# Optimization experiments

Hardware: AMD Instinct MI355X
Metric: run time of the kernel (lower is better)

Reference implementation:

```python
import jax, jax.numpy as jnp
import numpy as np

VQ_NUM = 3
EMB_NUM = 1024
COMMITMENT_WEIGHT = 1.0
# cumprod of [1, emb_num, emb_num] -> per-stage index bases
CUMPROD = [1, EMB_NUM, EMB_NUM * EMB_NUM]


def setup_inputs() -> dict:
    key = jax.random.key(0)
    k0, k1, k2, k3 = jax.random.split(key, 4)
    z = jax.random.normal(k0, (8, 4096, 512), dtype=jnp.float32)
    # linear_in: nn.Linear(in_ch=512, emb_ch=256, bias=False) -> weight [emb_ch, in_ch]
    W_in = jax.random.normal(k1, (VQ_NUM, 256, 512), dtype=jnp.float32) * 0.02
    # linear_out: nn.Linear(emb_ch=256, in_ch=512, bias=False) -> weight [in_ch, emb_ch]
    W_out = jax.random.normal(k2, (VQ_NUM, 512, 256), dtype=jnp.float32) * 0.02
    # one codebook per stage (share_residual_codebooks=False)
    codebooks = jax.random.normal(k3, (VQ_NUM, EMB_NUM, 256), dtype=jnp.float32) * 0.02
    return {"z": z, "W_in": W_in, "W_out": W_out, "codebooks": codebooks}


def reference(z, W_in, W_out, codebooks):
    sg = jax.lax.stop_gradient
    z_q = jnp.zeros_like(z)
    r = z
    loss = jnp.float32(0.0)
    index_sum = jnp.zeros(z.shape[:2], dtype=jnp.int64 if jax.config.jax_enable_x64 else jnp.int32)
    for i in range(VQ_NUM):
        # linear_in
        zi = jnp.einsum('bnc,ec->bne', r, W_in[i])  # [B,N,emb_ch]
        v = codebooks[i]  # [S, emb_ch]
        # squared L2 distance: ||z||^2 + ||v||^2 - 2 z.v
        dist = (jnp.sum(zi * zi, axis=-1, keepdims=True)
                + jnp.sum(v * v, axis=-1)
                - 2.0 * jnp.einsum('bne,se->bns', zi, v))  # [B,N,S]
        idx = jnp.argmin(dist, axis=-1)  # [B,N] int
        zq = v[idx]  # codebook lookup, [B,N,emb_ch]
        loss = loss + (COMMITMENT_WEIGHT * jnp.mean((sg(zq) - zi) ** 2)
                       + jnp.mean((zq - sg(zi)) ** 2))
        # straight-through estimator
        zq_ste = zi + sg(zq - zi)
        # linear_out
        r_q = jnp.einsum('bne,ce->bnc', zq_ste, W_out[i])  # [B,N,in_ch]
        index_sum = index_sum + idx.astype(index_sum.dtype) * CUMPROD[i]
        z_q = z_q + r_q
        r = z - sg(z_q)
    loss = loss / VQ_NUM + jnp.mean((z_q - z) ** 2)
    return z_q, index_sum, loss
```

## Files before the change

### kernel.cpp

```cpp
#include <hip/hip_runtime.h>

#define MTOK 32768
#define CIN  512
#define EMB  256
#define NCODE 1024
#define VQ   3
#define DELTA 2e-3f

typedef short s16x8 __attribute__((ext_vector_type(8)));
typedef float f32x4 __attribute__((ext_vector_type(4)));
typedef unsigned short u16;

static __device__ __forceinline__ u16 f2bf(float x) {
    unsigned int u = __float_as_uint(x);
    u += 0x7FFF + ((u >> 16) & 1);
    return (u16)(u >> 16);
}
static __device__ __forceinline__ float bf2f(u16 h) {
    return __uint_as_float(((unsigned int)h) << 16);
}

__global__ void init_k(double* loss_acc, int* cnt) {
    loss_acc[0] = 0.0;
    loss_acc[1] = 0.0;
    #pragma unroll
    for (int i = 0; i < 8; ++i) cnt[i] = 0;
}

__global__ __launch_bounds__(64) void prep_cb_k(const float* __restrict__ cbs,
                                                double* __restrict__ vnorm64,
                                                float* __restrict__ vnorm32,
                                                u16* __restrict__ cbh,
                                                u16* __restrict__ cbl) {
    int s = blockIdx.x;
    const float* row = cbs + (size_t)s * EMB;
    double acc = 0.0;
    for (int k = threadIdx.x; k < EMB; k += 64) {
        float v = row[k];
        double vd = (double)v; acc += vd * vd;
        u16 h = f2bf(v);
        u16 l = f2bf(v - bf2f(h));
        cbh[(size_t)s * EMB + k] = h;
        cbl[(size_t)s * EMB + k] = l;
    }
    #pragma unroll
    for (int off = 32; off > 0; off >>= 1) acc += __shfl_down(acc, off, 64);
    if (threadIdx.x == 0) { vnorm64[s] = acc; vnorm32[s] = (float)acc; }
}

__global__ __launch_bounds__(256) void prep_w_k(const float* __restrict__ W_in,
                                                u16* __restrict__ wh,
                                                u16* __restrict__ wl) {
    int i = blockIdx.x * 256 + threadIdx.x;
    float v = W_in[i];
    u16 h = f2bf(v);
    wh[i] = h;
    wl[i] = f2bf(v - bf2f(h));
}

__global__ __launch_bounds__(256) void prep_wt_k(const float* __restrict__ W_in,
                                                 float* __restrict__ WinT) {
    int i = blockIdx.x * 256 + threadIdx.x;
    int s = i / (EMB * CIN);
    int rem = i - s * (EMB * CIN);
    int e = rem / CIN;
    int k = rem - e * CIN;
    WinT[(size_t)s * CIN * EMB + (size_t)k * EMB + e] = W_in[i];
}

__global__ __launch_bounds__(256) void prep_T_k(const float* __restrict__ cbs,
                                                const float* __restrict__ Wout,
                                                float* __restrict__ T) {
    const int stage = blockIdx.z;
    const float* A = cbs  + (size_t)stage * NCODE * EMB;
    const float* B = Wout + (size_t)stage * CIN * EMB;
    float* C = T + (size_t)stage * NCODE * CIN;
    __shared__ float As[64][33];
    __shared__ float Bs[64][33];
    const int tid = threadIdx.x;
    const int ty = tid >> 4, tx = tid & 15;
    const int m0 = blockIdx.x * 64;
    const int n0 = blockIdx.y * 64;
    const int lrow = tid >> 5, lcol = tid & 31;
    double acc[4][4];
    #pragma unroll
    for (int i = 0; i < 4; ++i)
        #pragma unroll
        for (int j = 0; j < 4; ++j) acc[i][j] = 0.0;

    for (int k0 = 0; k0 < EMB; k0 += 32) {
        __syncthreads();
        #pragma unroll
        for (int t = 0; t < 8; ++t) {
            int r = lrow + 8 * t;
            As[r][lcol] = A[(size_t)(m0 + r) * EMB + k0 + lcol];
            Bs[r][lcol] = B[(size_t)(n0 + r) * EMB + k0 + lcol];
        }
        __syncthreads();
        #pragma unroll
        for (int k = 0; k < 32; ++k) {
            double a[4], b[4];
            #pragma unroll
            for (int i = 0; i < 4; ++i) a[i] = (double)As[ty * 4 + i][k];
            #pragma unroll
            for (int j = 0; j < 4; ++j) b[j] = (double)Bs[tx * 4 + j][k];
            #pragma unroll
            for (int i = 0; i < 4; ++i)
                #pragma unroll
                for (int j = 0; j < 4; ++j) acc[i][j] += a[i] * b[j];
        }
    }
    #pragma unroll
    for (int i = 0; i < 4; ++i) {
        float4 v = make_float4((float)acc[i][0], (float)acc[i][1],
                               (float)acc[i][2], (float)acc[i][3]);
        *reinterpret_cast<float4*>(&C[(size_t)(m0 + ty * 4 + i) * CIN + n0 + tx * 4]) = v;
    }
}

__global__ __launch_bounds__(256, 2) void zi_mfma_k(const float* __restrict__ z,
                                                    const float* __restrict__ zq,
                                                    const u16* __restrict__ wh,
                                                    const u16* __restrict__ wl,
                                                    float* __restrict__ zi,
                                                    double* __restrict__ loss_acc,
                                                    int stage0) {
    __shared__ __align__(16) u16 swh[2][16][520];
    __shared__ __align__(16) u16 swl[2][16][520];
    const int tid = threadIdx.x;
    const int w = tid >> 6;
    const int l = tid & 63;
    const int col = l & 15;
    const int g = l >> 4;
    const int mw = blockIdx.x * 64 + w * 16;
    const int sr = tid >> 4, sq = tid & 15;

    s16x8 ah[16], al[16];
    {
        const float* zr = z  + (size_t)(mw + col) * CIN + g * 8;
        const float* qr = zq + (size_t)(mw + col) * CIN + g * 8;
        #pragma unroll
        for (int kc = 0; kc < 16; ++kc) {
            float4 f0 = *reinterpret_cast<const float4*>(zr + kc * 32);
            float4 f1 = *reinterpret_cast<const float4*>(zr + kc * 32 + 4);
            float f[8] = {f0.x, f0.y, f0.z, f0.w, f1.x, f1.y, f1.z, f1.w};
            if (!stage0) {
                float4 q0 = *reinterpret_cast<const float4*>(qr + kc * 32);
                float4 q1 = *reinterpret_cast<const float4*>(qr + kc * 32 + 4);
                f[0] -= q0.x; f[1] -= q0.y; f[2] -= q0.z; f[3] -= q0.w;
                f[4] -= q1.x; f[5] -= q1.y; f[6] -= q1.z; f[7] -= q1.w;
            }
            #pragma unroll
            for (int j = 0; j < 8; ++j) {
                u16 h = f2bf(f[j]);
                u16 lo = f2bf(f[j] - bf2f(h));
                ah[kc][j] = (short)h; al[kc][j] = (short)lo;
            }
        }
    }

    const u16* gh = wh + (size_t)sr * CIN + sq * 8;
    const u16* gl = wl + (size_t)sr * CIN + sq * 8;
    uint4 h0, h1, h2, h3, l0, l1, l2, l3;
#define ZLOAD(NT) do { const u16* th = gh + (size_t)(NT) * (16 * CIN);                \
    const u16* tl = gl + (size_t)(NT) * (16 * CIN);                                   \
    h0 = *(const uint4*)(th);        h1 = *(const uint4*)(th + 128);                  \
    h2 = *(const uint4*)(th + 256);  h3 = *(const uint4*)(th + 384);                  \
    l0 = *(const uint4*)(tl);        l1 = *(const uint4*)(tl + 128);                  \
    l2 = *(const uint4*)(tl + 256);  l3 = *(const uint4*)(tl + 384); } while (0)
#define ZWRITE(P) do {                                                                \
    *(uint4*)&swh[P][sr][sq * 8]       = h0;  *(uint4*)&swh[P][sr][sq * 8 + 128] = h1;\
    *(uint4*)&swh[P][sr][sq * 8 + 256] = h2;  *(uint4*)&swh[P][sr][sq * 8 + 384] = h3;\
    *(uint4*)&swl[P][sr][sq * 8]       = l0;  *(uint4*)&swl[P][sr][sq * 8 + 128] = l1;\
    *(uint4*)&swl[P][sr][sq * 8 + 256] = l2;  *(uint4*)&swl[P][sr][sq * 8 + 384] = l3;\
    } while (0)
    ZLOAD(0); ZWRITE(0); ZLOAD(1);

    double zn = 0.0;
    for (int nt = 0; nt < 16; ++nt) {
        __syncthreads();
        const int p = nt & 1;
        if (nt + 1 < 16) ZWRITE((nt + 1) & 1);
        if (nt + 2 < 16) ZLOAD(nt + 2);
        f32x4 a0 = {0.f, 0.f, 0.f, 0.f};
        f32x4 a1 = {0.f, 0.f, 0.f, 0.f};
        f32x4 a2 = {0.f, 0.f, 0.f, 0.f};
        #pragma unroll
        for (int kc = 0; kc < 16; ++kc) {
            s16x8 Bh = *(const s16x8*)&swh[p][col][g * 8 + kc * 32];
            s16x8 Bl = *(const s16x8*)&swl[p][col][g * 8 + kc * 32];
            a0 = __builtin_amdgcn_mfma_f32_16x16x32_bf16(ah[kc], Bh, a0, 0, 0, 0);
            a1 = __builtin_amdgcn_mfma_f32_16x16x32_bf16(al[kc], Bh, a1, 0, 0, 0);
            a2 = __builtin_amdgcn_mfma_f32_16x16x32_bf16(ah[kc], Bl, a2, 0, 0, 0);
        }
        #pragma unroll
        for (int r = 0; r < 4; ++r) {
            float v = a0[r] + a1[r] + a2[r];
            zi[(size_t)(mw + g * 4 + r) * EMB + nt * 16 + col] = v;
            zn += (double)v * (double)v;
        }
    }
#undef ZLOAD
#undef ZWRITE
    #pragma unroll
    for (int off = 32; off > 0; off >>= 1) zn += __shfl_down(zn, off, 64);
    if (l == 0) atomicAdd(loss_acc, zn);
}

__global__ __launch_bounds__(256, 2) void pref_k(const float* __restrict__ zi,
                                                 const u16* __restrict__ cbh,
                                                 const u16* __restrict__ cbl,
                                                 const float* __restrict__ vnorm32,
                                                 int* __restrict__ idx,
                                                 int* __restrict__ idx_sum,
                                                 float* __restrict__ mind,
                                                 int* __restrict__ flagged,
                                                 int* __restrict__ cnt,
                                                 int* __restrict__ fullList,
                                                 int* __restrict__ cntF,
                                                 int* __restrict__ cand2,
                                                 double* __restrict__ loss_acc,
                                                 int stage0, int cumprod) {
    __shared__ __align__(16) u16 sbh[2][16][264];
    __shared__ __align__(16) u16 sbl[2][16][264];
    __shared__ double loss_s[16];
    const int tid = threadIdx.x;
    const int w = tid >> 6;
    const int l = tid & 63;
    const int col = l & 15;
    const int g = l >> 4;
    const int mw = blockIdx.x * 64 + w * 16;
    const int sr = tid >> 4, sq = tid & 15;

    s16x8 ah[8], al[8];
    {
        const float* zr = zi + (size_t)(mw + col) * EMB + g * 8;
        #pragma unroll
        for (int kc = 0; kc < 8; ++kc) {
            float4 f0 = *reinterpret_cast<const float4*>(zr + kc * 32);
            float4 f1 = *reinterpret_cast<const float4*>(zr + kc * 32 + 4);
            float f[8] = {f0.x, f0.y, f0.z, f0.w, f1.x, f1.y, f1.z, f1.w};
            #pragma unroll
            for (int j = 0; j < 8; ++j) {
                u16 h = f2bf(f[j]);
                u16 lo = f2bf(f[j] - bf2f(h));
                ah[kc][j] = (short)h;
                al[kc][j] = (short)lo;
            }
        }
    }

    float b1[4] = {1e30f, 1e30f, 1e30f, 1e30f};
    float b2[4] = {1e30f, 1e30f, 1e30f, 1e30f};
    float b3[4] = {1e30f, 1e30f, 1e30f, 1e30f};
    int   i1[4] = {0, 0, 0, 0};
    int   i2[4] = {0, 0, 0, 0};

    const u16* gh = cbh + (size_t)sr * EMB + sq * 8;
    const u16* gl = cbl + (size_t)sr * EMB + sq * 8;
    uint4 h0, h1, l0, l1;
#define PLOAD(CT) do { const u16* th = gh + (size_t)(CT) * (16 * EMB);                \
    const u16* tl = gl + (size_t)(CT) * (16 * EMB);                                   \
    h0 = *(const uint4*)(th);  h1 = *(const uint4*)(th + 128);                        \
    l0 = *(const uint4*)(tl);  l1 = *(const uint4*)(tl + 128); } while (0)
#define PWRITE(P) do {                                                                \
    *(uint4*)&sbh[P][sr][sq * 8] = h0;  *(uint4*)&sbh[P][sr][sq * 8 + 128] = h1;      \
    *(uint4*)&sbl[P][sr][sq * 8] = l0;  *(uint4*)&sbl[P][sr][sq * 8 + 128] = l1;      \
    } while (0)
    PLOAD(0); PWRITE(0); PLOAD(1);

    for (int ct = 0; ct < 64; ++ct) {
        __syncthreads();
        const int p = ct & 1;
        if (ct + 1 < 64) PWRITE((ct + 1) & 1);
        if (ct + 2 < 64) PLOAD(ct + 2);
        const float vn = vnorm32[ct * 16 + col];
        f32x4 a0 = {0.f, 0.f, 0.f, 0.f};
        f32x4 a1 = {0.f, 0.f, 0.f, 0.f};
        f32x4 a2 = {0.f, 0.f, 0.f, 0.f};
        #pragma unroll
        for (int kc = 0; kc < 8; ++kc) {
            s16x8 Bh = *(const s16x8*)&sbh[p][col][g * 8 + kc * 32];
            s16x8 Bl = *(const s16x8*)&sbl[p][col][g * 8 + kc * 32];
            a0 = __builtin_amdgcn_mfma_f32_16x16x32_bf16(ah[kc], Bh, a0, 0, 0, 0);
            a1 = __builtin_amdgcn_mfma_f32_16x16x32_bf16(al[kc], Bh, a1, 0, 0, 0);
            a2 = __builtin_amdgcn_mfma_f32_16x16x32_bf16(ah[kc], Bl, a2, 0, 0, 0);
        }
        #pragma unroll
        for (int r = 0; r < 4; ++r) {
            float sc = vn - 2.f * (a0[r] + a1[r] + a2[r]);
            int c = ct * 16 + col;
            if (sc < b1[r]) { b3[r] = b2[r]; b2[r] = b1[r]; i2[r] = i1[r]; b1[r] = sc; i1[r] = c; }
            else if (sc < b2[r]) { b3[r] = b2[r]; b2[r] = sc; i2[r] = c; }
            else b3[r] = fminf(b3[r], sc);
        }
    }
#undef PLOAD
#undef PWRITE

    #pragma unroll
    for (int off = 1; off < 16; off <<= 1) {
        #pragma unroll
        for (int r = 0; r < 4; ++r) {
            float c1 = __shfl_xor(b1[r], off, 64);
            int   j1 = __shfl_xor(i1[r], off, 64);
            float c2 = __shfl_xor(b2[r], off, 64);
            int   j2 = __shfl_xor(i2[r], off, 64);
            float c3 = __shfl_xor(b3[r], off, 64);
            float nb1, nb2, nb3; int ni1, ni2;
            if (c1 < b1[r] || (c1 == b1[r] && j1 < i1[r])) {
                nb1 = c1; ni1 = j1;
                if (b1[r] < c2 || (b1[r] == c2 && i1[r] < j2)) {
                    nb2 = b1[r]; ni2 = i1[r]; nb3 = fminf(b2[r], c2);
                } else {
                    nb2 = c2; ni2 = j2; nb3 = fminf(b1[r], c3);
                }
            } else {
                nb1 = b1[r]; ni1 = i1[r];
                if (c1 < b2[r] || (c1 == b2[r] && j1 < i2[r])) {
                    nb2 = c1; ni2 = j1; nb3 = fminf(b2[r], c2);
                } else {
                    nb2 = b2[r]; ni2 = i2[r]; nb3 = fminf(c1, b3[r]);
                }
            }
            b1[r] = nb1; b2[r] = nb2; b3[r] = nb3; i1[r] = ni1; i2[r] = ni2;
        }
    }
    if (col == 0) {
        double lsum = 0.0;
        #pragma unroll
        for (int r = 0; r < 4; ++r) {
            int m = mw + g * 4 + r;
            idx[m] = i1[r];
            if (stage0) idx_sum[m] = i1[r];
            else        idx_sum[m] += i1[r] * cumprod;
            mind[m] = b1[r];
            lsum += (double)b1[r];
            if (b2[r] - b1[r] < DELTA) {
                if (b3[r] - b1[r] < DELTA) {
                    int slot = atomicAdd(cntF, 1);
                    fullList[slot] = m;
                } else {
                    int slot = atomicAdd(cnt, 1);
                    flagged[slot] = m;
                    cand2[m] = i2[r];
                }
            }
        }
        loss_s[w * 4 + g] = lsum;
    }
    __syncthreads();
    if (tid == 0) {
        double s = 0.0;
        #pragma unroll
        for (int q = 0; q < 16; ++q) s += loss_s[q];
        atomicAdd(loss_acc, s);
    }
}

__global__ __launch_bounds__(256) void rescan_pair_k(const float* __restrict__ z,
                                                     const float* __restrict__ zqv,
                                                     const float* __restrict__ WinT,
                                                     const float* __restrict__ cb,
                                                     const double* __restrict__ vnorm64,
                                                     const int* __restrict__ flagged,
                                                     const int* __restrict__ cnt,
                                                     const int* __restrict__ cand2,
                                                     int* __restrict__ idx,
                                                     int* __restrict__ idx_sum,
                                                     float* __restrict__ mind,
                                                     double* __restrict__ loss_acc,
                                                     int cumprod, int stage0) {
    __shared__ double r64[8][CIN];
    __shared__ int mArr[8], cAArr[8], cBArr[8];
    double* zi_l = &r64[0][0];
    const int tid = threadIdx.x;
    const int w = tid >> 6, l = tid & 63;
    const int n = *cnt;

    for (int jb = blockIdx.x; jb * 8 < n; jb += gridDim.x) {
        const int nt = min(8, n - jb * 8);
        __syncthreads();
        if (tid < nt) {
            int m = flagged[jb * 8 + tid];
            mArr[tid] = m;
            cAArr[tid] = idx[m]; cBArr[tid] = cand2[m];
        }
        __syncthreads();
        for (int t = 0; t < nt; ++t) {
            const int m = mArr[t];
            #pragma unroll
            for (int h = 0; h < 2; ++h) {
                int k = tid + h * 256;
                float rv = z[(size_t)m * CIN + k];
                if (!stage0) rv -= zqv[(size_t)m * CIN + k];
                r64[t][k] = (double)rv;
            }
        }
        __syncthreads();
        double acc[8] = {0, 0, 0, 0, 0, 0, 0, 0};
        #pragma unroll 4
        for (int k = 0; k < CIN; ++k) {
            double wv = (double)WinT[(size_t)k * EMB + tid];
            #pragma unroll
            for (int t = 0; t < 8; ++t) acc[t] += r64[t][k] * wv;
        }
        __syncthreads();
        #pragma unroll
        for (int t = 0; t < 8; ++t) zi_l[t * 256 + tid] = acc[t];
        __syncthreads();

        for (int t = w; t < nt; t += 4) {
            const int cA = cAArr[t], cB = cBArr[t], m = mArr[t];
            const double* zt = zi_l + t * 256;
            float4 vA = *(const float4*)(cb + (size_t)cA * EMB + 4 * l);
            float4 vB = *(const float4*)(cb + (size_t)cB * EMB + 4 * l);
            double z0 = zt[4 * l], z1 = zt[4 * l + 1];
            double z2 = zt[4 * l + 2], z3 = zt[4 * l + 3];
            double sA = z0 * (double)vA.x + z1 * (double)vA.y
                      + z2 * (double)vA.z + z3 * (double)vA.w;
            double sB = z0 * (double)vB.x + z1 * (double)vB.y
                      + z2 * (double)vB.z + z3 * (double)vB.w;
            #pragma unroll
            for (int off = 1; off < 64; off <<= 1) {
                sA += __shfl_xor(sA, off, 64);
                sB += __shfl_xor(sB, off, 64);
            }
            if (l == 0) {
                double dA = vnorm64[cA] - 2.0 * sA;
                double dB = vnorm64[cB] - 2.0 * sB;
                int bi; double best;
                if (dB < dA || (dB == dA && cB < cA)) { bi = cB; best = dB; }
                else                                   { bi = cA; best = dA; }
                int oldI = idx[m];
                if (bi != oldI) { idx[m] = bi; idx_sum[m] += (bi - oldI) * cumprod; }
                atomicAdd(loss_acc, best - (double)mind[m]);
                mind[m] = (float)best;
            }
        }
    }
}

__global__ __launch_bounds__(256) void fullscan_k(const float* __restrict__ z,
                                                  const float* __restrict__ zqv,
                                                  const float* __restrict__ WinT,
                                                  const float* __restrict__ cb,
                                                  const double* __restrict__ vnorm64,
                                                  const int* __restrict__ fullList,
                                                  const int* __restrict__ cntF,
                                                  int* __restrict__ idx,
                                                  int* __restrict__ idx_sum,
                                                  float* __restrict__ mind,
                                                  double* __restrict__ loss_acc,
                                                  int cumprod, int stage0) {
    __shared__ double r64[CIN];
    __shared__ double zi64[EMB];
    __shared__ double sred[256];
    __shared__ int ired[256];
    const int tid = threadIdx.x;
    const int n = *cntF;

    for (int j = blockIdx.x; j < n; j += gridDim.x) {
        const int m = fullList[j];
        __syncthreads();
        #pragma unroll
        for (int h = 0; h < 2; ++h) {
            int k = tid + h * 256;
            float rv = z[(size_t)m * CIN + k];
            if (!stage0) rv -= zqv[(size_t)m * CIN + k];
            r64[k] = (double)rv;
        }
        __syncthreads();
        {
            double acc = 0.0;
            #pragma unroll 8
            for (int k = 0; k < CIN; ++k)
                acc += r64[k] * (double)WinT[(size_t)k * EMB + tid];
            zi64[tid] = acc;
        }
        __syncthreads();
        double best = 1e300; int bi = 0;
        #pragma unroll
        for (int q = 0; q < 4; ++q) {
            const int c = q * 256 + tid;
            const float* row = cb + (size_t)c * EMB;
            double s0 = 0, s1 = 0, s2 = 0, s3 = 0;
            #pragma unroll 4
            for (int e = 0; e < EMB; e += 4) {
                float4 v = *(const float4*)(row + e);
                s0 += zi64[e]     * (double)v.x;
                s1 += zi64[e + 1] * (double)v.y;
                s2 += zi64[e + 2] * (double)v.z;
                s3 += zi64[e + 3] * (double)v.w;
            }
            double sc = vnorm64[c] - 2.0 * ((s0 + s1) + (s2 + s3));
            if (sc < best) { best = sc; bi = c; }
        }
        sred[tid] = best; ired[tid] = bi;
        __syncthreads();
        for (int off = 128; off > 0; off >>= 1) {
            if (tid < off) {
                double ob = sred[tid + off]; int oi = ired[tid + off];
                if (ob < sred[tid] || (ob == sred[tid] && oi < ired[tid])) {
                    sred[tid] = ob; ired[tid] = oi;
                }
            }
            __syncthreads();
        }
        if (tid == 0) {
            int oldI = idx[m], bi2 = ired[0];
            double best2 = sred[0];
            if (bi2 != oldI) { idx[m] = bi2; idx_sum[m] += (bi2 - oldI) * cumprod; }
            atomicAdd(loss_acc, best2 - (double)mind[m]);
            mind[m] = (float)best2;
        }
    }
}

__global__ __launch_bounds__(256) void gather_k(const float* __restrict__ T,
                                                const int* __restrict__ idx,
                                                const float* __restrict__ z,
                                                float* __restrict__ zq,
                                                int stage0, int last,
                                                double* __restrict__ loss_acc) {
    __shared__ double red[256];
    int m = blockIdx.x * 16 + (threadIdx.x >> 4);
    int q = threadIdx.x & 15;
    const float* src = T + (size_t)idx[m] * CIN;
    float* dst = zq + (size_t)m * CIN;
    double s = 0.0;
    #pragma unroll
    for (int it = 0; it < 8; ++it) {
        int off = it * 64 + q * 4;
        float4 t = *reinterpret_cast<const float4*>(src + off);
        if (!stage0) {
            float4 o = *reinterpret_cast<const float4*>(dst + off);
            t.x += o.x; t.y += o.y; t.z += o.z; t.w += o.w;
        }
        *reinterpret_cast<float4*>(dst + off) = t;
        if (last) {
            float4 zv = *reinterpret_cast<const float4*>(z + (size_t)m * CIN + off);
            double d0 = (double)zv.x - (double)t.x;
            double d1 = (double)zv.y - (double)t.y;
            double d2 = (double)zv.z - (double)t.z;
            double d3 = (double)zv.w - (double)t.w;
            s += d0 * d0 + d1 * d1 + d2 * d2 + d3 * d3;
        }
    }
    if (last) {
        red[threadIdx.x] = s;
        __syncthreads();
        for (int off = 128; off > 0; off >>= 1) {
            if (threadIdx.x < off) red[threadIdx.x] += red[threadIdx.x + off];
            __syncthreads();
        }
        if (threadIdx.x == 0) atomicAdd(loss_acc + 1, red[0]);
    }
}

__global__ void final_k(const int* __restrict__ idx_sum,
                        const double* __restrict__ loss_acc,
                        float* __restrict__ out) {
    int i = blockIdx.x * blockDim.x + threadIdx.x;
    if (i < MTOK) out[MTOK * CIN + i] = (float)idx_sum[i];
    if (i == 0) {
        double loss = 2.0 * loss_acc[0] / (3.0 * (double)MTOK * (double)EMB)
                    + loss_acc[1] / ((double)MTOK * (double)CIN);
        out[MTOK * CIN + MTOK] = (float)loss;
    }
}

extern "C" void kernel_launch(void* const* d_in, const int* in_sizes, int n_in,
                              void* d_out, int out_size, void* d_ws, size_t ws_size,
                              hipStream_t stream) {
    const float* z     = (const float*)d_in[0];
    const float* W_in  = (const float*)d_in[1];
    const float* W_out = (const float*)d_in[2];
    const float* cbs   = (const float*)d_in[3];
    float* out = (float*)d_out;
    char* ws = (char*)d_ws;

    double* vnorm64  = (double*)ws;
    double* loss_acc = (double*)(ws + 24576);
    int*    cnt      = (int*)(ws + 24592);
    float*  vnorm32  = (float*)(ws + 24624);
    u16*    cbh      = (u16*)(ws + 36912);
    u16*    cbl      = (u16*)(ws + 1609776);
    u16*    wh       = (u16*)(ws + 3182640);
    u16*    wl       = (u16*)(ws + 3969072);
    float*  WinT     = (float*)(ws + 4755504);
    float*  T        = (float*)(ws + 6328368);
    float*  zi       = (float*)(ws + 12619824);
    char*   p        = ws + 46174256;
    int*    idx      = (int*)p;
    int*    idx_sum  = (int*)(p + 131072);
    int*    flagged  = (int*)(p + 262144);
    float*  mind     = (float*)(p + 393216);
    int*    cand2    = (int*)(p + 524288);
    int*    fullList = (int*)(p + 655360);

    float* zq = out;

    init_k<<<dim3(1), dim3(1), 0, stream>>>(loss_acc, cnt);
    prep_cb_k<<<dim3(VQ * NCODE), dim3(64), 0, stream>>>(cbs, vnorm64, vnorm32, cbh, cbl);
    prep_w_k<<<dim3(VQ * EMB * CIN / 256), dim3(256), 0, stream>>>(W_in, wh, wl);
    prep_wt_k<<<dim3(VQ * EMB * CIN / 256), dim3(256), 0, stream>>>(W_in, WinT);
    prep_T_k<<<dim3(NCODE / 64, CIN / 64, VQ), dim3(256), 0, stream>>>(cbs, W_out, T);

    const int cumprod[VQ] = {1, 1024, 1024 * 1024};
    for (int i = 0; i < VQ; ++i) {
        const float* cb = cbs + (size_t)i * NCODE * EMB;
        zi_mfma_k<<<dim3(MTOK / 64), dim3(256), 0, stream>>>(
            z, zq, wh + (size_t)i * EMB * CIN, wl + (size_t)i * EMB * CIN,
            zi, loss_acc, i == 0 ? 1 : 0);
        pref_k<<<dim3(MTOK / 64), dim3(256), 0, stream>>>(
            zi, cbh + (size_t)i * NCODE * EMB, cbl + (size_t)i * NCODE * EMB,
            vnorm32 + i * NCODE, idx, idx_sum, mind, flagged, cnt + i,
            fullList, cnt + 3 + i, cand2, loss_acc, i == 0 ? 1 : 0, cumprod[i]);
        rescan_pair_k<<<dim3(512), dim3(256), 0, stream>>>(
            z, zq, WinT + (size_t)i * EMB * CIN, cb, vnorm64 + i * NCODE,
            flagged, cnt + i, cand2, idx, idx_sum, mind, loss_acc, cumprod[i],
            i == 0 ? 1 : 0);
        fullscan_k<<<dim3(256), dim3(256), 0, stream>>>(
            z, zq, WinT + (size_t)i * EMB * CIN, cb, vnorm64 + i * NCODE,
            fullList, cnt + 3 + i, idx, idx_sum, mind, loss_acc, cumprod[i],
            i == 0 ? 1 : 0);
        gather_k<<<dim3(MTOK / 16), dim3(256), 0, stream>>>(
            T + (size_t)i * NCODE * CIN, idx, z, zq, i == 0 ? 1 : 0,
            i == VQ - 1 ? 1 : 0, loss_acc);
    }
    final_k<<<dim3(MTOK / 256), dim3(256), 0, stream>>>(idx_sum, loss_acc, out);
}
```

Before: 936.4 us.

## Process two 16-row token tiles per wave in pref_k to reuse codebook tiles

```diff
diff --git a/kernel.cpp b/kernel.cpp
--- a/kernel.cpp
+++ b/kernel.cpp
@@ -207,7 +207,7 @@
     if (l == 0) atomicAdd(loss_acc, zn);
 }
 
-__global__ __launch_bounds__(256, 2) void pref_k(const float* __restrict__ zi,
+__global__ __launch_bounds__(256, 1) void pref_k(const float* __restrict__ zi,
                                                  const u16* __restrict__ cbh,
                                                  const u16* __restrict__ cbl,
                                                  const float* __restrict__ vnorm32,
@@ -229,32 +229,45 @@
     const int l = tid & 63;
     const int col = l & 15;
     const int g = l >> 4;
-    const int mw = blockIdx.x * 64 + w * 16;
+    const int mw = blockIdx.x * 128 + w * 32;
     const int sr = tid >> 4, sq = tid & 15;
 
-    s16x8 ah[8], al[8];
+    s16x8 ah0[8], al0[8], ah1[8], al1[8];
     {
-        const float* zr = zi + (size_t)(mw + col) * EMB + g * 8;
+        const float* zr0 = zi + (size_t)(mw + col) * EMB + g * 8;
+        const float* zr1 = zi + (size_t)(mw + 16 + col) * EMB + g * 8;
         #pragma unroll
         for (int kc = 0; kc < 8; ++kc) {
-            float4 f0 = *reinterpret_cast<const float4*>(zr + kc * 32);
-            float4 f1 = *reinterpret_cast<const float4*>(zr + kc * 32 + 4);
+            float4 f0 = *reinterpret_cast<const float4*>(zr0 + kc * 32);
+            float4 f1 = *reinterpret_cast<const float4*>(zr0 + kc * 32 + 4);
             float f[8] = {f0.x, f0.y, f0.z, f0.w, f1.x, f1.y, f1.z, f1.w};
             #pragma unroll
             for (int j = 0; j < 8; ++j) {
                 u16 h = f2bf(f[j]);
                 u16 lo = f2bf(f[j] - bf2f(h));
-                ah[kc][j] = (short)h;
-                al[kc][j] = (short)lo;
-            }
-        }
-    }
-
-    float b1[4] = {1e30f, 1e30f, 1e30f, 1e30f};
-    float b2[4] = {1e30f, 1e30f, 1e30f, 1e30f};
-    float b3[4] = {1e30f, 1e30f, 1e30f, 1e30f};
-    int   i1[4] = {0, 0, 0, 0};
-    int   i2[4] = {0, 0, 0, 0};
+                ah0[kc][j] = (short)h;
+                al0[kc][j] = (short)lo;
+            }
+            float4 e0 = *reinterpret_cast<const float4*>(zr1 + kc * 32);
+            float4 e1 = *reinterpret_cast<const float4*>(zr1 + kc * 32 + 4);
+            float e[8] = {e0.x, e0.y, e0.z, e0.w, e1.x, e1.y, e1.z, e1.w};
+            #pragma unroll
+            for (int j = 0; j < 8; ++j) {
+                u16 h = f2bf(e[j]);
+                u16 lo = f2bf(e[j] - bf2f(h));
+                ah1[kc][j] = (short)h;
+                al1[kc][j] = (short)lo;
+            }
+        }
+    }
+
+    float b1a[4], b2a[4], b3a[4], b1b[4], b2b[4], b3b[4];
+    int   i1a[4], i2a[4], i1b[4], i2b[4];
+    #pragma unroll
+    for (int r = 0; r < 4; ++r) {
+        b1a[r] = b2a[r] = b3a[r] = 1e30f; i1a[r] = i2a[r] = 0;
+        b1b[r] = b2b[r] = b3b[r] = 1e30f; i1b[r] = i2b[r] = 0;
+    }
 
     const u16* gh = cbh + (size_t)sr * EMB + sq * 8;
     const u16* gl = cbl + (size_t)sr * EMB + sq * 8;
@@ -275,75 +288,103 @@
         if (ct + 1 < 64) PWRITE((ct + 1) & 1);
         if (ct + 2 < 64) PLOAD(ct + 2);
         const float vn = vnorm32[ct * 16 + col];
-        f32x4 a0 = {0.f, 0.f, 0.f, 0.f};
-        f32x4 a1 = {0.f, 0.f, 0.f, 0.f};
-        f32x4 a2 = {0.f, 0.f, 0.f, 0.f};
+        f32x4 a00 = {0.f, 0.f, 0.f, 0.f}, a01 = {0.f, 0.f, 0.f, 0.f}, a02 = {0.f, 0.f, 0.f, 0.f};
+        f32x4 a10 = {0.f, 0.f, 0.f, 0.f}, a11 = {0.f, 0.f, 0.f, 0.f}, a12 = {0.f, 0.f, 0.f, 0.f};
         #pragma unroll
         for (int kc = 0; kc < 8; ++kc) {
             s16x8 Bh = *(const s16x8*)&sbh[p][col][g * 8 + kc * 32];
             s16x8 Bl = *(const s16x8*)&sbl[p][col][g * 8 + kc * 32];
-            a0 = __builtin_amdgcn_mfma_f32_16x16x32_bf16(ah[kc], Bh, a0, 0, 0, 0);
-            a1 = __builtin_amdgcn_mfma_f32_16x16x32_bf16(al[kc], Bh, a1, 0, 0, 0);
-            a2 = __builtin_amdgcn_mfma_f32_16x16x32_bf16(ah[kc], Bl, a2, 0, 0, 0);
+            a00 = __builtin_amdgcn_mfma_f32_16x16x32_bf16(ah0[kc], Bh, a00, 0, 0, 0);
+            a10 = __builtin_amdgcn_mfma_f32_16x16x32_bf16(ah1[kc], Bh, a10, 0, 0, 0);
+            a01 = __builtin_amdgcn_mfma_f32_16x16x32_bf16(al0[kc], Bh, a01, 0, 0, 0);
+            a11 = __builtin_amdgcn_mfma_f32_16x16x32_bf16(al1[kc], Bh, a11, 0, 0, 0);
+            a02 = __builtin_amdgcn_mfma_f32_16x16x32_bf16(ah0[kc], Bl, a02, 0, 0, 0);
+            a12 = __builtin_amdgcn_mfma_f32_16x16x32_bf16(ah1[kc], Bl, a12, 0, 0, 0);
         }
         #pragma unroll
         for (int r = 0; r < 4; ++r) {
-            float sc = vn - 2.f * (a0[r] + a1[r] + a2[r]);
             int c = ct * 16 + col;
-            if (sc < b1[r]) { b3[r] = b2[r]; b2[r] = b1[r]; i2[r] = i1[r]; b1[r] = sc; i1[r] = c; }
-            else if (sc < b2[r]) { b3[r] = b2[r]; b2[r] = sc; i2[r] = c; }
-            else b3[r] = fminf(b3[r], sc);
+            float sa = vn - 2.f * (a00[r] + a01[r] + a02[r]);
+            if (sa < b1a[r]) { b3a[r] = b2a[r]; b2a[r] = b1a[r]; i2a[r] = i1a[r]; b1a[r] = sa; i1a[r] = c; }
+            else if (sa < b2a[r]) { b3a[r] = b2a[r]; b2a[r] = sa; i2a[r] = c; }
+            else b3a[r] = fminf(b3a[r], sa);
+            float sb = vn - 2.f * (a10[r] + a11[r] + a12[r]);
+            if (sb < b1b[r]) { b3b[r] = b2b[r]; b2b[r] = b1b[r]; i2b[r] = i1b[r]; b1b[r] = sb; i1b[r] = c; }
+            else if (sb < b2b[r]) { b3b[r] = b2b[r]; b2b[r] = sb; i2b[r] = c; }
+            else b3b[r] = fminf(b3b[r], sb);
         }
     }
 #undef PLOAD
 #undef PWRITE
 
-    #pragma unroll
-    for (int off = 1; off < 16; off <<= 1) {
-        #pragma unroll
-        for (int r = 0; r < 4; ++r) {
-            float c1 = __shfl_xor(b1[r], off, 64);
-            int   j1 = __shfl_xor(i1[r], off, 64);
-            float c2 = __shfl_xor(b2[r], off, 64);
-            int   j2 = __shfl_xor(i2[r], off, 64);
-            float c3 = __shfl_xor(b3[r], off, 64);
-            float nb1, nb2, nb3; int ni1, ni2;
-            if (c1 < b1[r] || (c1 == b1[r] && j1 < i1[r])) {
-                nb1 = c1; ni1 = j1;
-                if (b1[r] < c2 || (b1[r] == c2 && i1[r] < j2)) {
-                    nb2 = b1[r]; ni2 = i1[r]; nb3 = fminf(b2[r], c2);
-                } else {
-                    nb2 = c2; ni2 = j2; nb3 = fminf(b1[r], c3);
-                }
-            } else {
-                nb1 = b1[r]; ni1 = i1[r];
-                if (c1 < b2[r] || (c1 == b2[r] && j1 < i2[r])) {
-                    nb2 = c1; ni2 = j1; nb3 = fminf(b2[r], c2);
-                } else {
-                    nb2 = b2[r]; ni2 = i2[r]; nb3 = fminf(c1, b3[r]);
-                }
-            }
-            b1[r] = nb1; b2[r] = nb2; b3[r] = nb3; i1[r] = ni1; i2[r] = ni2;
-        }
-    }
+#define MERGE16(B1, B2, B3, I1, I2) do {                                              \
+    _Pragma("unroll")                                                                 \
+    for (int off = 1; off < 16; off <<= 1) {                                          \
+        _Pragma("unroll")                                                             \
+        for (int r = 0; r < 4; ++r) {                                                 \
+            float c1 = __shfl_xor(B1[r], off, 64);                                    \
+            int   j1 = __shfl_xor(I1[r], off, 64);                                    \
+            float c2 = __shfl_xor(B2[r], off, 64);                                    \
+            int   j2 = __shfl_xor(I2[r], off, 64);                                    \
+            float c3 = __shfl_xor(B3[r], off, 64);                                    \
+            float nb1, nb2, nb3; int ni1, ni2;                                        \
+            if (c1 < B1[r] || (c1 == B1[r] && j1 < I1[r])) {                          \
+                nb1 = c1; ni1 = j1;                                                   \
+                if (B1[r] < c2 || (B1[r] == c2 && I1[r] < j2)) {                      \
+                    nb2 = B1[r]; ni2 = I1[r]; nb3 = fminf(B2[r], c2);                 \
+                } else {                                                              \
+                    nb2 = c2; ni2 = j2; nb3 = fminf(B1[r], c3);                       \
+                }                                                                     \
+            } else {                                                                  \
+                nb1 = B1[r]; ni1 = I1[r];                                             \
+                if (c1 < B2[r] || (c1 == B2[r] && j1 < I2[r])) {                      \
+                    nb2 = c1; ni2 = j1; nb3 = fminf(B2[r], c2);                       \
+                } else {                                                              \
+                    nb2 = B2[r]; ni2 = I2[r]; nb3 = fminf(c1, B3[r]);                 \
+                }                                                                     \
+            }                                                                         \
+            B1[r] = nb1; B2[r] = nb2; B3[r] = nb3; I1[r] = ni1; I2[r] = ni2;          \
+        }                                                                             \
+    }                                                                                 \
+} while (0)
+    MERGE16(b1a, b2a, b3a, i1a, i2a);
+    MERGE16(b1b, b2b, b3b, i1b, i2b);
+#undef MERGE16
+
     if (col == 0) {
         double lsum = 0.0;
         #pragma unroll
         for (int r = 0; r < 4; ++r) {
             int m = mw + g * 4 + r;
-            idx[m] = i1[r];
-            if (stage0) idx_sum[m] = i1[r];
-            else        idx_sum[m] += i1[r] * cumprod;
-            mind[m] = b1[r];
-            lsum += (double)b1[r];
-            if (b2[r] - b1[r] < DELTA) {
-                if (b3[r] - b1[r] < DELTA) {
+            idx[m] = i1a[r];
+            if (stage0) idx_sum[m] = i1a[r];
+            else        idx_sum[m] += i1a[r] * cumprod;
+            mind[m] = b1a[r];
+            lsum += (double)b1a[r];
+            if (b2a[r] - b1a[r] < DELTA) {
+                if (b3a[r] - b1a[r] < DELTA) {
                     int slot = atomicAdd(cntF, 1);
                     fullList[slot] = m;
                 } else {
                     int slot = atomicAdd(cnt, 1);
                     flagged[slot] = m;
-                    cand2[m] = i2[r];
+                    cand2[m] = i2a[r];
+                }
+            }
+            int m2 = mw + 16 + g * 4 + r;
+            idx[m2] = i1b[r];
+            if (stage0) idx_sum[m2] = i1b[r];
+            else        idx_sum[m2] += i1b[r] * cumprod;
+            mind[m2] = b1b[r];
+            lsum += (double)b1b[r];
+            if (b2b[r] - b1b[r] < DELTA) {
+                if (b3b[r] - b1b[r] < DELTA) {
+                    int slot = atomicAdd(cntF, 1);
+                    fullList[slot] = m2;
+                } else {
+                    int slot = atomicAdd(cnt, 1);
+                    flagged[slot] = m2;
+                    cand2[m2] = i2b[r];
                 }
             }
         }
@@ -613,7 +654,7 @@
         zi_mfma_k<<<dim3(MTOK / 64), dim3(256), 0, stream>>>(
             z, zq, wh + (size_t)i * EMB * CIN, wl + (size_t)i * EMB * CIN,
             zi, loss_acc, i == 0 ? 1 : 0);
-        pref_k<<<dim3(MTOK / 64), dim3(256), 0, stream>>>(
+        pref_k<<<dim3(MTOK / 128), dim3(256), 0, stream>>>(
             zi, cbh + (size_t)i * NCODE * EMB, cbl + (size_t)i * NCODE * EMB,
             vnorm32 + i * NCODE, idx, idx_sum, mind, flagged, cnt + i,
             fullList, cnt + 3 + i, cand2, loss_acc, i == 0 ? 1 : 0, cumprod[i]);
```

After: 1.028 ms. 1.1x slower.

## Fuse linear_in MFMA projection into codebook prefilter kernel with packed bf16 split

Applied to the files above, without the earlier changes.

```diff
diff --git a/kernel.cpp b/kernel.cpp
--- a/kernel.cpp
+++ b/kernel.cpp
@@ -10,6 +10,7 @@
 typedef short s16x8 __attribute__((ext_vector_type(8)));
 typedef float f32x4 __attribute__((ext_vector_type(4)));
 typedef unsigned short u16;
+typedef unsigned int u32;
 
 static __device__ __forceinline__ u16 f2bf(float x) {
     unsigned int u = __float_as_uint(x);
@@ -118,109 +119,24 @@
     }
 }
 
-__global__ __launch_bounds__(256, 2) void zi_mfma_k(const float* __restrict__ z,
-                                                    const float* __restrict__ zq,
-                                                    const u16* __restrict__ wh,
-                                                    const u16* __restrict__ wl,
-                                                    float* __restrict__ zi,
-                                                    double* __restrict__ loss_acc,
-                                                    int stage0) {
-    __shared__ __align__(16) u16 swh[2][16][520];
-    __shared__ __align__(16) u16 swl[2][16][520];
-    const int tid = threadIdx.x;
-    const int w = tid >> 6;
-    const int l = tid & 63;
-    const int col = l & 15;
-    const int g = l >> 4;
-    const int mw = blockIdx.x * 64 + w * 16;
-    const int sr = tid >> 4, sq = tid & 15;
-
-    s16x8 ah[16], al[16];
-    {
-        const float* zr = z  + (size_t)(mw + col) * CIN + g * 8;
-        const float* qr = zq + (size_t)(mw + col) * CIN + g * 8;
-        #pragma unroll
-        for (int kc = 0; kc < 16; ++kc) {
-            float4 f0 = *reinterpret_cast<const float4*>(zr + kc * 32);
-            float4 f1 = *reinterpret_cast<const float4*>(zr + kc * 32 + 4);
-            float f[8] = {f0.x, f0.y, f0.z, f0.w, f1.x, f1.y, f1.z, f1.w};
-            if (!stage0) {
-                float4 q0 = *reinterpret_cast<const float4*>(qr + kc * 32);
-                float4 q1 = *reinterpret_cast<const float4*>(qr + kc * 32 + 4);
-                f[0] -= q0.x; f[1] -= q0.y; f[2] -= q0.z; f[3] -= q0.w;
-                f[4] -= q1.x; f[5] -= q1.y; f[6] -= q1.z; f[7] -= q1.w;
-            }
-            #pragma unroll
-            for (int j = 0; j < 8; ++j) {
-                u16 h = f2bf(f[j]);
-                u16 lo = f2bf(f[j] - bf2f(h));
-                ah[kc][j] = (short)h; al[kc][j] = (short)lo;
-            }
-        }
-    }
-
-    const u16* gh = wh + (size_t)sr * CIN + sq * 8;
-    const u16* gl = wl + (size_t)sr * CIN + sq * 8;
-    uint4 h0, h1, h2, h3, l0, l1, l2, l3;
-#define ZLOAD(NT) do { const u16* th = gh + (size_t)(NT) * (16 * CIN);                \
-    const u16* tl = gl + (size_t)(NT) * (16 * CIN);                                   \
-    h0 = *(const uint4*)(th);        h1 = *(const uint4*)(th + 128);                  \
-    h2 = *(const uint4*)(th + 256);  h3 = *(const uint4*)(th + 384);                  \
-    l0 = *(const uint4*)(tl);        l1 = *(const uint4*)(tl + 128);                  \
-    l2 = *(const uint4*)(tl + 256);  l3 = *(const uint4*)(tl + 384); } while (0)
-#define ZWRITE(P) do {                                                                \
-    *(uint4*)&swh[P][sr][sq * 8]       = h0;  *(uint4*)&swh[P][sr][sq * 8 + 128] = h1;\
-    *(uint4*)&swh[P][sr][sq * 8 + 256] = h2;  *(uint4*)&swh[P][sr][sq * 8 + 384] = h3;\
-    *(uint4*)&swl[P][sr][sq * 8]       = l0;  *(uint4*)&swl[P][sr][sq * 8 + 128] = l1;\
-    *(uint4*)&swl[P][sr][sq * 8 + 256] = l2;  *(uint4*)&swl[P][sr][sq * 8 + 384] = l3;\
-    } while (0)
-    ZLOAD(0); ZWRITE(0); ZLOAD(1);
-
-    double zn = 0.0;
-    for (int nt = 0; nt < 16; ++nt) {
-        __syncthreads();
-        const int p = nt & 1;
-        if (nt + 1 < 16) ZWRITE((nt + 1) & 1);
-        if (nt + 2 < 16) ZLOAD(nt + 2);
-        f32x4 a0 = {0.f, 0.f, 0.f, 0.f};
-        f32x4 a1 = {0.f, 0.f, 0.f, 0.f};
-        f32x4 a2 = {0.f, 0.f, 0.f, 0.f};
-        #pragma unroll
-        for (int kc = 0; kc < 16; ++kc) {
-            s16x8 Bh = *(const s16x8*)&swh[p][col][g * 8 + kc * 32];
-            s16x8 Bl = *(const s16x8*)&swl[p][col][g * 8 + kc * 32];
-            a0 = __builtin_amdgcn_mfma_f32_16x16x32_bf16(ah[kc], Bh, a0, 0, 0, 0);
-            a1 = __builtin_amdgcn_mfma_f32_16x16x32_bf16(al[kc], Bh, a1, 0, 0, 0);
-            a2 = __builtin_amdgcn_mfma_f32_16x16x32_bf16(ah[kc], Bl, a2, 0, 0, 0);
-        }
-        #pragma unroll
-        for (int r = 0; r < 4; ++r) {
-            float v = a0[r] + a1[r] + a2[r];
-            zi[(size_t)(mw + g * 4 + r) * EMB + nt * 16 + col] = v;
-            zn += (double)v * (double)v;
-        }
-    }
-#undef ZLOAD
-#undef ZWRITE
-    #pragma unroll
-    for (int off = 32; off > 0; off >>= 1) zn += __shfl_down(zn, off, 64);
-    if (l == 0) atomicAdd(loss_acc, zn);
-}
-
-__global__ __launch_bounds__(256, 2) void pref_k(const float* __restrict__ zi,
-                                                 const u16* __restrict__ cbh,
-                                                 const u16* __restrict__ cbl,
-                                                 const float* __restrict__ vnorm32,
-                                                 int* __restrict__ idx,
-                                                 int* __restrict__ idx_sum,
-                                                 float* __restrict__ mind,
-                                                 int* __restrict__ flagged,
-                                                 int* __restrict__ cnt,
-                                                 int* __restrict__ fullList,
-                                                 int* __restrict__ cntF,
-                                                 int* __restrict__ cand2,
-                                                 double* __restrict__ loss_acc,
-                                                 int stage0, int cumprod) {
+__global__ __launch_bounds__(256, 2) void fused_k(const float* __restrict__ z,
+                                                  const float* __restrict__ zq,
+                                                  const u16* __restrict__ wh,
+                                                  const u16* __restrict__ wl,
+                                                  const u16* __restrict__ cbh,
+                                                  const u16* __restrict__ cbl,
+                                                  const float* __restrict__ vnorm32,
+                                                  u32* __restrict__ zi_hl,
+                                                  int* __restrict__ idx,
+                                                  int* __restrict__ idx_sum,
+                                                  float* __restrict__ mind,
+                                                  int* __restrict__ flagged,
+                                                  int* __restrict__ cnt,
+                                                  int* __restrict__ fullList,
+                                                  int* __restrict__ cntF,
+                                                  int* __restrict__ cand2,
+                                                  double* __restrict__ loss_acc,
+                                                  int stage0, int cumprod) {
     __shared__ __align__(16) u16 sbh[2][16][264];
     __shared__ __align__(16) u16 sbl[2][16][264];
     __shared__ double loss_s[16];
@@ -232,20 +148,95 @@
     const int mw = blockIdx.x * 64 + w * 16;
     const int sr = tid >> 4, sq = tid & 15;
 
-    s16x8 ah[8], al[8];
     {
-        const float* zr = zi + (size_t)(mw + col) * EMB + g * 8;
-        #pragma unroll
-        for (int kc = 0; kc < 8; ++kc) {
+        s16x8 ah[16], al[16];
+        const float* zr = z  + (size_t)(mw + col) * CIN + g * 8;
+        const float* qr = zq + (size_t)(mw + col) * CIN + g * 8;
+        #pragma unroll
+        for (int kc = 0; kc < 16; ++kc) {
             float4 f0 = *reinterpret_cast<const float4*>(zr + kc * 32);
             float4 f1 = *reinterpret_cast<const float4*>(zr + kc * 32 + 4);
             float f[8] = {f0.x, f0.y, f0.z, f0.w, f1.x, f1.y, f1.z, f1.w};
+            if (!stage0) {
+                float4 q0 = *reinterpret_cast<const float4*>(qr + kc * 32);
+                float4 q1 = *reinterpret_cast<const float4*>(qr + kc * 32 + 4);
+                f[0] -= q0.x; f[1] -= q0.y; f[2] -= q0.z; f[3] -= q0.w;
+                f[4] -= q1.x; f[5] -= q1.y; f[6] -= q1.z; f[7] -= q1.w;
+            }
             #pragma unroll
             for (int j = 0; j < 8; ++j) {
                 u16 h = f2bf(f[j]);
                 u16 lo = f2bf(f[j] - bf2f(h));
-                ah[kc][j] = (short)h;
-                al[kc][j] = (short)lo;
+                ah[kc][j] = (short)h; al[kc][j] = (short)lo;
+            }
+        }
+
+        const u16* gwh = wh + (size_t)sr * CIN + sq * 8;
+        const u16* gwl = wl + (size_t)sr * CIN + sq * 8;
+        uint4 h0, h1, h2, h3, l0, l1, l2, l3;
+#define WLOAD(NT) do { const u16* th = gwh + (size_t)(NT) * (16 * CIN);               \
+    const u16* tl = gwl + (size_t)(NT) * (16 * CIN);                                  \
+    h0 = *(const uint4*)(th);        h1 = *(const uint4*)(th + 128);                  \
+    h2 = *(const uint4*)(th + 256);  h3 = *(const uint4*)(th + 384);                  \
+    l0 = *(const uint4*)(tl);        l1 = *(const uint4*)(tl + 128);                  \
+    l2 = *(const uint4*)(tl + 256);  l3 = *(const uint4*)(tl + 384); } while (0)
+#define WWRITE() do {                                                                 \
+    *(uint4*)&sbh[0][sr][sq * 8]       = h0;  *(uint4*)&sbh[0][sr][sq * 8 + 128] = h1;\
+    *(uint4*)&sbh[1][sr][sq * 8]       = h2;  *(uint4*)&sbh[1][sr][sq * 8 + 128] = h3;\
+    *(uint4*)&sbl[0][sr][sq * 8]       = l0;  *(uint4*)&sbl[0][sr][sq * 8 + 128] = l1;\
+    *(uint4*)&sbl[1][sr][sq * 8]       = l2;  *(uint4*)&sbl[1][sr][sq * 8 + 128] = l3;\
+    } while (0)
+        WLOAD(0);
+
+        double zn = 0.0;
+        for (int nt = 0; nt < 16; ++nt) {
+            __syncthreads();
+            WWRITE();
+            __syncthreads();
+            if (nt + 1 < 16) WLOAD(nt + 1);
+            f32x4 a0 = {0.f, 0.f, 0.f, 0.f};
+            f32x4 a1 = {0.f, 0.f, 0.f, 0.f};
+            f32x4 a2 = {0.f, 0.f, 0.f, 0.f};
+            #pragma unroll
+            for (int kc = 0; kc < 16; ++kc) {
+                const int p = kc >> 3;
+                const int ko = (kc & 7) * 32 + g * 8;
+                s16x8 Bh = *(const s16x8*)&sbh[p][col][ko];
+                s16x8 Bl = *(const s16x8*)&sbl[p][col][ko];
+                a0 = __builtin_amdgcn_mfma_f32_16x16x32_bf16(ah[kc], Bh, a0, 0, 0, 0);
+                a1 = __builtin_amdgcn_mfma_f32_16x16x32_bf16(al[kc], Bh, a1, 0, 0, 0);
+                a2 = __builtin_amdgcn_mfma_f32_16x16x32_bf16(ah[kc], Bl, a2, 0, 0, 0);
+            }
+            #pragma unroll
+            for (int r = 0; r < 4; ++r) {
+                float v = a0[r] + a1[r] + a2[r];
+                u16 h = f2bf(v);
+                u16 lo = f2bf(v - bf2f(h));
+                zi_hl[(size_t)(mw + g * 4 + r) * EMB + nt * 16 + col] =
+                    (u32)h | ((u32)lo << 16);
+                zn += (double)v * (double)v;
+            }
+        }
+#undef WLOAD
+#undef WWRITE
+        #pragma unroll
+        for (int off = 32; off > 0; off >>= 1) zn += __shfl_down(zn, off, 64);
+        if (l == 0) atomicAdd(loss_acc, zn);
+    }
+    __syncthreads();
+
+    s16x8 ah[8], al[8];
+    {
+        const u32* zr = zi_hl + (size_t)(mw + col) * EMB + g * 8;
+        #pragma unroll
+        for (int kc = 0; kc < 8; ++kc) {
+            uint4 u0 = *reinterpret_cast<const uint4*>(zr + kc * 32);
+            uint4 u1 = *reinterpret_cast<const uint4*>(zr + kc * 32 + 4);
+            u32 u[8] = {u0.x, u0.y, u0.z, u0.w, u1.x, u1.y, u1.z, u1.w};
+            #pragma unroll
+            for (int j = 0; j < 8; ++j) {
+                ah[kc][j] = (short)(u[j] & 0xffffu);
+                al[kc][j] = (short)(u[j] >> 16);
             }
         }
     }
@@ -590,7 +581,7 @@
     u16*    wl       = (u16*)(ws + 3969072);
     float*  WinT     = (float*)(ws + 4755504);
     float*  T        = (float*)(ws + 6328368);
-    float*  zi       = (float*)(ws + 12619824);
+    u32*    zi_hl    = (u32*)(ws + 12619824);
     char*   p        = ws + 46174256;
     int*    idx      = (int*)p;
     int*    idx_sum  = (int*)(p + 131072);
@@ -610,12 +601,10 @@
     const int cumprod[VQ] = {1, 1024, 1024 * 1024};
     for (int i = 0; i < VQ; ++i) {
         const float* cb = cbs + (size_t)i * NCODE * EMB;
-        zi_mfma_k<<<dim3(MTOK / 64), dim3(256), 0, stream>>>(
+        fused_k<<<dim3(MTOK / 64), dim3(256), 0, stream>>>(
             z, zq, wh + (size_t)i * EMB * CIN, wl + (size_t)i * EMB * CIN,
-            zi, loss_acc, i == 0 ? 1 : 0);
-        pref_k<<<dim3(MTOK / 64), dim3(256), 0, stream>>>(
-            zi, cbh + (size_t)i * NCODE * EMB, cbl + (size_t)i * NCODE * EMB,
-            vnorm32 + i * NCODE, idx, idx_sum, mind, flagged, cnt + i,
+            cbh + (size_t)i * NCODE * EMB, cbl + (size_t)i * NCODE * EMB,
+            vnorm32 + i * NCODE, zi_hl, idx, idx_sum, mind, flagged, cnt + i,
             fullList, cnt + 3 + i, cand2, loss_acc, i == 0 ? 1 : 0, cumprod[i]);
         rescan_pair_k<<<dim3(512), dim3(256), 0, stream>>>(
             z, zq, WinT + (size_t)i * EMB * CIN, cb, vnorm64 + i * NCODE,
```

After: 876.2 us. -6.4%, faster.
